# Kernel tuning notes

Hardware: AMD Instinct MI355X
Metric: run time of the kernel (lower is better)

The kernel has to match this reference:

```python
import jax, jax.numpy as jnp
import numpy as np

GROUPS = 32
K = 5          # up_kernel_size
UP = 2         # up_factor
EPS = 1e-5


def group_norm(x, w, b):
    B, C, H, W = x.shape
    xr = x.reshape(B, GROUPS, -1)
    mu = xr.mean(axis=2, keepdims=True)
    var = xr.var(axis=2, keepdims=True)
    xr = (xr - mu) * jax.lax.rsqrt(var + EPS)
    return xr.reshape(B, C, H, W) * w[None, :, None, None] + b[None, :, None, None]


def setup_inputs() -> dict:
    key = jax.random.key(0)
    ks = jax.random.split(key, 4)
    B, Cy, Cx, E, H, W = 4, 256, 256, 32, 64, 64
    return {
        "y": jax.random.normal(ks[0], (B, Cy, H * UP, W * UP), jnp.float32),
        "x": jax.random.normal(ks[1], (B, Cx, H, W), jnp.float32),
        "gn_y_w": jnp.ones((Cy,), jnp.float32),
        "gn_y_b": jnp.zeros((Cy,), jnp.float32),
        "gn_x_w": jnp.ones((Cx,), jnp.float32),
        "gn_x_b": jnp.zeros((Cx,), jnp.float32),
        "q_w": jax.random.normal(ks[2], (E, Cy), jnp.float32) * 0.02,
        "q_b": jnp.zeros((E,), jnp.float32),
        "k_w": jax.random.normal(ks[3], (E, Cx), jnp.float32) * 0.02,
        "k_b": jnp.zeros((E,), jnp.float32),
    }


def reference(y, x, gn_y_w, gn_y_b, gn_x_w, gn_x_b, q_w, q_b, k_w, k_b):
    pad = K // 2
    yn = group_norm(y, gn_y_w, gn_y_b)
    xn = group_norm(x, gn_x_w, gn_x_b)
    # 1x1 convs
    q = jnp.einsum('bchw,ec->behw', yn, q_w) + q_b[None, :, None, None]  # [B,E,Hu,Wu]
    k = jnp.einsum('bchw,ec->behw', xn, k_w) + k_b[None, :, None, None]  # [B,E,H,W]
    B, E, H, W = k.shape
    C = x.shape[1]
    # view q as per-low-res-cell blocks of UPxUP high-res queries
    q_r = q.reshape(B, E, H, UP, W, UP)
    k_pad = jnp.pad(k, ((0, 0), (0, 0), (pad, pad), (pad, pad)))  # zero pad (out-of-range -> 0 logit)
    v_pad = jnp.pad(x, ((0, 0), (0, 0), (pad, pad), (pad, pad)))
    # qk: logits over the KxK window (loop over 25 fixed offsets, vectorized inside)
    logits = []
    for dy in range(K):
        for dx in range(K):
            ks = k_pad[:, :, dy:dy + H, dx:dx + W]            # [B,E,H,W]
            logits.append(jnp.einsum('behuwv,behw->bhuwv', q_r, ks))
    logits = jnp.stack(logits, axis=1)                        # [B,KK,H,u,W,u]
    attn = jax.nn.softmax(logits, axis=1)
    # av: weighted aggregation of v over the same window
    out = jnp.zeros((B, C, H, UP, W, UP), x.dtype)
    idx = 0
    for dy in range(K):
        for dx in range(K):
            vs = v_pad[:, :, dy:dy + H, dx:dx + W]            # [B,C,H,W]
            out = out + attn[:, idx][:, None] * vs[:, :, :, None, :, None]
            idx += 1
    return out.reshape(B, C, H * UP, W * UP)
```

## Files before the change

### kernel.cpp

```cpp
#include <hip/hip_runtime.h>

#define EPSV 1e-5f

__global__ __launch_bounds__(256) void stats_kernel(const float* __restrict__ y,
                                                    const float* __restrict__ x,
                                                    float* __restrict__ part) {
    int bid = blockIdx.x;
    const float* src = (bid < 1024) ? (y + (size_t)bid * 16384)
                                    : (x + (size_t)(bid - 1024) * 16384);
    const float4* p = (const float4*)src;
    float s = 0.f, ss = 0.f;
    #pragma unroll 8
    for (int i = threadIdx.x; i < 4096; i += 256) {
        float4 v = p[i];
        s  += v.x + v.y + v.z + v.w;
        ss += v.x*v.x + v.y*v.y + v.z*v.z + v.w*v.w;
    }
    for (int off = 32; off > 0; off >>= 1) {
        s  += __shfl_down(s, off);
        ss += __shfl_down(ss, off);
    }
    __shared__ float red[8];
    int wid = threadIdx.x >> 6, lane = threadIdx.x & 63;
    if (lane == 0) { red[wid*2] = s; red[wid*2+1] = ss; }
    __syncthreads();
    if (threadIdx.x == 0) {
        part[bid*2+0] = red[0] + red[2] + red[4] + red[6];
        part[bid*2+1] = red[1] + red[3] + red[5] + red[7];
    }
}

__global__ __launch_bounds__(64) void make_eff_kernel(const float* __restrict__ qw, const float* __restrict__ qb,
                                                      const float* __restrict__ gyw, const float* __restrict__ gyb,
                                                      const float* __restrict__ kw, const float* __restrict__ kb,
                                                      const float* __restrict__ gxw, const float* __restrict__ gxb,
                                                      const float* __restrict__ part,
                                                      float* __restrict__ WeffQ, float* __restrict__ beffQ,
                                                      float* __restrict__ WeffK, float* __restrict__ beffK) {
    int id = blockIdx.x;
    int isK = id >> 7, b = (id >> 5) & 3, e = id & 31;
    const float* w     = isK ? kw  : qw;
    const float* bias  = isK ? kb  : qb;
    const float* gamma = isK ? gxw : gyw;
    const float* beta  = isK ? gxb : gyb;
    float inv_n = isK ? (1.f/32768.f) : (1.f/131072.f);
    float* W  = isK ? WeffK : WeffQ;
    float* be = isK ? beffK : beffQ;
    float partial = 0.f;
    for (int c = threadIdx.x; c < 256; c += 64) {
        int g = c >> 3, grp = b*32 + g;
        float s = 0.f, ss = 0.f;
        if (isK) {
            #pragma unroll
            for (int k2 = 0; k2 < 2; ++k2) {
                s  += part[(1024 + grp*2 + k2)*2 + 0];
                ss += part[(1024 + grp*2 + k2)*2 + 1];
            }
        } else {
            #pragma unroll
            for (int k2 = 0; k2 < 8; ++k2) {
                s  += part[(grp*8 + k2)*2 + 0];
                ss += part[(grp*8 + k2)*2 + 1];
            }
        }
        float mu = s * inv_n;
        float rs = rsqrtf(fmaf(-mu, mu, ss * inv_n) + EPSV);
        float wc = w[e*256 + c];
        float weff = wc * gamma[c] * rs;
        W[((size_t)b*256 + c)*32 + e] = weff;
        partial += wc * beta[c] - weff * mu;
    }
    for (int off = 32; off > 0; off >>= 1) partial += __shfl_down(partial, off);
    if (threadIdx.x == 0) be[b*32 + e] = partial + bias[e];
}

__global__ __launch_bounds__(256) void proj_kernel(const float* __restrict__ y, const float* __restrict__ x,
                                                   const float* __restrict__ WeffQ, const float* __restrict__ beffQ,
                                                   const float* __restrict__ WeffK, const float* __restrict__ beffK,
                                                   float* __restrict__ qbuf, float* __restrict__ kbuf) {
    int bid = blockIdx.x;
    int isX = bid >= 512;
    int lb = isX ? bid - 512 : bid;
    int b    = isX ? (lb >> 5) : (lb >> 7);
    int pxb  = isX ? (lb & 31) : (lb & 127);
    int npix = isX ? 4096 : 16384;
    const float* src   = isX ? x : y;
    const float* WeffT = isX ? WeffK : WeffQ;
    const float* beff  = isX ? beffK : beffQ;
    float* dst = isX ? kbuf : qbuf;

    int pix0 = pxb * 128 + (threadIdx.x & 63) * 2;
    int eg = __builtin_amdgcn_readfirstlane(threadIdx.x >> 6);
    const float* wp = WeffT + (size_t)b*256*32 + eg*8;
    float acc[2][8];
    #pragma unroll
    for (int j = 0; j < 8; ++j) {
        float bv = beff[b*32 + eg*8 + j];
        acc[0][j] = bv; acc[1][j] = bv;
    }
    const float* ysrc = src + (size_t)b*256*npix + pix0;
    #pragma unroll 8
    for (int c = 0; c < 256; ++c) {
        float2 t = *(const float2*)(ysrc + (size_t)c*npix);
        #pragma unroll
        for (int j = 0; j < 8; ++j) {
            float wj = wp[c*32 + j];
            acc[0][j] = fmaf(t.x, wj, acc[0][j]);
            acc[1][j] = fmaf(t.y, wj, acc[1][j]);
        }
    }
    float* dbase = dst + ((size_t)b*npix + pix0)*32 + eg*8;
    #pragma unroll
    for (int px = 0; px < 2; ++px) {
        float4 o0 = {acc[px][0], acc[px][1], acc[px][2], acc[px][3]};
        float4 o1 = {acc[px][4], acc[px][5], acc[px][6], acc[px][7]};
        *(float4*)(dbase + px*32 + 0) = o0;
        *(float4*)(dbase + px*32 + 4) = o1;
    }
}

__global__ __launch_bounds__(256) void attn_weights_kernel(const float* __restrict__ q,
                                                           const float* __restrict__ kk,
                                                           float* __restrict__ g_attn)
{
    __shared__ __align__(16) float sK[5184];
    __shared__ __align__(16) float sA[6400];
    int h0 = blockIdx.y * 8, w0 = blockIdx.x * 8;
    int b = blockIdx.z;
    int tid = threadIdx.x;

    for (int i = tid; i < 1152; i += 256) {
        int pos = i >> 3, e4 = i & 7;
        int r = pos / 12, c = pos - 12*r;
        int gh = h0 + r - 2, gw = w0 + c - 2;
        float4 v = make_float4(0.f, 0.f, 0.f, 0.f);
        if (gh >= 0 && gh < 64 && gw >= 0 && gw < 64)
            v = *(const float4*)(kk + (((size_t)b*4096 + gh*64 + gw)*32 + e4*4));
        *(float4*)&sK[pos*36 + e4*4] = v;
    }

    int h = tid >> 5, u = (tid >> 4) & 1, w = (tid >> 1) & 7, v = tid & 1;

    float qv[32];
    {
        int hh = 2*(h0 + h) + u, ww = 2*(w0 + w) + v;
        const float4* qp = (const float4*)(q + (((size_t)b*16384 + hh*128 + ww)*32));
        #pragma unroll
        for (int i4 = 0; i4 < 8; ++i4) {
            float4 t = qp[i4];
            qv[i4*4+0]=t.x; qv[i4*4+1]=t.y; qv[i4*4+2]=t.z; qv[i4*4+3]=t.w;
        }
    }
    __syncthreads();

    float a[25];
    const float* kbase = &sK[(h*12 + w)*36];
    #pragma unroll
    for (int j = 0; j < 25; ++j) {
        int dy = j / 5, dx = j - 5*dy;
        const float4* kp = (const float4*)(kbase + (dy*12 + dx)*36);
        float acc = 0.f;
        #pragma unroll
        for (int e4 = 0; e4 < 8; ++e4) {
            float4 kv = kp[e4];
            acc = fmaf(qv[e4*4+0], kv.x, acc);
            acc = fmaf(qv[e4*4+1], kv.y, acc);
            acc = fmaf(qv[e4*4+2], kv.z, acc);
            acc = fmaf(qv[e4*4+3], kv.w, acc);
        }
        a[j] = acc;
    }
    {
        float m = -1e30f;
        #pragma unroll
        for (int j = 0; j < 25; ++j) m = fmaxf(m, a[j]);
        float s = 0.f;
        #pragma unroll
        for (int j = 0; j < 25; ++j) { a[j] = __expf(a[j] - m); s += a[j]; }
        float inv = 1.f / s;
        #pragma unroll
        for (int j = 0; j < 25; ++j) sA[j*256 + tid] = a[j] * inv;
    }
    __syncthreads();

    float4* gdst = (float4*)(g_attn + ((size_t)b*64 + blockIdx.y*8 + blockIdx.x)*6400);
    const float4* ssrc = (const float4*)sA;
    for (int i = tid; i < 1600; i += 256) gdst[i] = ssrc[i];
}

__global__ __launch_bounds__(256) void gather_kernel(const float* __restrict__ g_attn,
                                                     const float* __restrict__ x,
                                                     float* __restrict__ out)
{
    __shared__ __align__(16) float sX[2880];
    int h0 = blockIdx.y * 8, w0 = blockIdx.x * 8;
    int b = blockIdx.z >> 4, chunk = blockIdx.z & 15;
    int tid = threadIdx.x;

    float a[25];
    {
        const float* abase = g_attn + ((size_t)b*64 + blockIdx.y*8 + blockIdx.x)*6400 + tid;
        #pragma unroll
        for (int j = 0; j < 25; ++j) a[j] = abase[j*256];
    }

    for (int i = 0; i < 9; ++i) {
        int t = i*256 + tid;
        int cc = t / 144, pos = t - 144*cc;
        int r = pos / 12, cl = pos - 12*r;
        int gh = h0 + r - 2, gw = w0 + cl - 2;
        float val = 0.f;
        if (gh >= 0 && gh < 64 && gw >= 0 && gw < 64)
            val = x[(((size_t)b*256 + chunk*16 + cc)*64 + gh)*64 + gw];
        sX[pos*20 + cc] = val;
    }

    int h = tid >> 5, u = (tid >> 4) & 1, w = (tid >> 1) & 7, v = tid & 1;
    int hh = 2*(h0 + h) + u, ww = 2*(w0 + w) + v;
    int vbase = (h*12 + w)*20;
    __syncthreads();

    #pragma unroll
    for (int g = 0; g < 4; ++g) {
        float o0 = 0.f, o1 = 0.f, o2 = 0.f, o3 = 0.f;
        const float* xb = &sX[vbase + g*4];
        #pragma unroll
        for (int j = 0; j < 25; ++j) {
            int dy = j / 5, dx = j - 5*dy;
            float4 xv = *(const float4*)(xb + (dy*12 + dx)*20);
            float aw = a[j];
            o0 = fmaf(aw, xv.x, o0);
            o1 = fmaf(aw, xv.y, o1);
            o2 = fmaf(aw, xv.z, o2);
            o3 = fmaf(aw, xv.w, o3);
        }
        size_t ob = (((size_t)b*256 + chunk*16 + g*4)*128 + hh)*128 + ww;
        out[ob]           = o0;
        out[ob + 16384]   = o1;
        out[ob + 32768]   = o2;
        out[ob + 49152]   = o3;
    }
}

extern "C" void kernel_launch(void* const* d_in, const int* in_sizes, int n_in,
                              void* d_out, int out_size, void* d_ws, size_t ws_size,
                              hipStream_t stream) {
    const float* y   = (const float*)d_in[0];
    const float* x   = (const float*)d_in[1];
    const float* gyw = (const float*)d_in[2];
    const float* gyb = (const float*)d_in[3];
    const float* gxw = (const float*)d_in[4];
    const float* gxb = (const float*)d_in[5];
    const float* qw  = (const float*)d_in[6];
    const float* qb  = (const float*)d_in[7];
    const float* kw  = (const float*)d_in[8];
    const float* kb  = (const float*)d_in[9];
    float* out = (float*)d_out;
    float* ws  = (float*)d_ws;

    float* part   = ws;
    float* WeffQ  = ws + 2560;
    float* beffQ  = ws + 35328;
    float* WeffK  = ws + 35456;
    float* beffK  = ws + 68224;
    float* qbuf   = ws + 68352;
    float* kbuf   = ws + 2165504;
    float* attnbf = ws + 2689792;

    stats_kernel<<<1280, 256, 0, stream>>>(y, x, part);
    make_eff_kernel<<<256, 64, 0, stream>>>(qw, qb, gyw, gyb, kw, kb, gxw, gxb,
                                            part, WeffQ, beffQ, WeffK, beffK);
    proj_kernel<<<640, 256, 0, stream>>>(y, x, WeffQ, beffQ, WeffK, beffK, qbuf, kbuf);
    attn_weights_kernel<<<dim3(8, 8, 4), 256, 0, stream>>>(qbuf, kbuf, attnbf);
    gather_kernel<<<dim3(8, 8, 64), 256, 0, stream>>>(attnbf, x, out);
}
```

Measured before the change: 204.2 us.

## Restructure projection to one pixel per thread and split attention dot over lanes

The projection kernel now uses 64-thread blocks where each thread computes all 32 output channels for one pixel. Each source element is loaded once and the weights become wave-uniform, replacing the earlier scheme of 8 channels by 2 pixels per thread. The attention-weights kernel doubles its threads per block, splits each 32-wide dot product across two half-waves and combines them with a cross-lane shuffle. It also writes softmax weights straight to global memory instead of staging them in shared memory. This is meant to add parallelism to the small 256-block attention launch and drop one LDS round trip and barrier, at the cost of more accumulator registers in the projection.

Result: slower. 221.1 us (+8.3%).

```diff
diff --git a/kernel.cpp b/kernel.cpp
--- a/kernel.cpp
+++ b/kernel.cpp
@@ -74,62 +74,54 @@
     if (threadIdx.x == 0) be[b*32 + e] = partial + bias[e];
 }
 
-__global__ __launch_bounds__(256) void proj_kernel(const float* __restrict__ y, const float* __restrict__ x,
-                                                   const float* __restrict__ WeffQ, const float* __restrict__ beffQ,
-                                                   const float* __restrict__ WeffK, const float* __restrict__ beffK,
-                                                   float* __restrict__ qbuf, float* __restrict__ kbuf) {
+__global__ __launch_bounds__(64) void proj_kernel(const float* __restrict__ y, const float* __restrict__ x,
+                                                  const float* __restrict__ WeffQ, const float* __restrict__ beffQ,
+                                                  const float* __restrict__ WeffK, const float* __restrict__ beffK,
+                                                  float* __restrict__ qbuf, float* __restrict__ kbuf) {
     int bid = blockIdx.x;
-    int isX = bid >= 512;
-    int lb = isX ? bid - 512 : bid;
-    int b    = isX ? (lb >> 5) : (lb >> 7);
-    int pxb  = isX ? (lb & 31) : (lb & 127);
+    int isX = bid >= 1024;
+    int lb  = isX ? bid - 1024 : bid;
+    int b   = isX ? (lb >> 6) : (lb >> 8);
+    int pxb = isX ? (lb & 63) : (lb & 255);
     int npix = isX ? 4096 : 16384;
     const float* src   = isX ? x : y;
     const float* WeffT = isX ? WeffK : WeffQ;
     const float* beff  = isX ? beffK : beffQ;
     float* dst = isX ? kbuf : qbuf;
 
-    int pix0 = pxb * 128 + (threadIdx.x & 63) * 2;
-    int eg = __builtin_amdgcn_readfirstlane(threadIdx.x >> 6);
-    const float* wp = WeffT + (size_t)b*256*32 + eg*8;
-    float acc[2][8];
-    #pragma unroll
-    for (int j = 0; j < 8; ++j) {
-        float bv = beff[b*32 + eg*8 + j];
-        acc[0][j] = bv; acc[1][j] = bv;
-    }
-    const float* ysrc = src + (size_t)b*256*npix + pix0;
-    #pragma unroll 8
+    int pix = pxb * 64 + threadIdx.x;
+    float acc[32];
+    #pragma unroll
+    for (int j = 0; j < 32; ++j) acc[j] = beff[b*32 + j];
+
+    const float* sp    = src + (size_t)b*256*npix + pix;
+    const float* wbase = WeffT + (size_t)b*256*32;
+    #pragma unroll 4
     for (int c = 0; c < 256; ++c) {
-        float2 t = *(const float2*)(ysrc + (size_t)c*npix);
-        #pragma unroll
-        for (int j = 0; j < 8; ++j) {
-            float wj = wp[c*32 + j];
-            acc[0][j] = fmaf(t.x, wj, acc[0][j]);
-            acc[1][j] = fmaf(t.y, wj, acc[1][j]);
-        }
-    }
-    float* dbase = dst + ((size_t)b*npix + pix0)*32 + eg*8;
-    #pragma unroll
-    for (int px = 0; px < 2; ++px) {
-        float4 o0 = {acc[px][0], acc[px][1], acc[px][2], acc[px][3]};
-        float4 o1 = {acc[px][4], acc[px][5], acc[px][6], acc[px][7]};
-        *(float4*)(dbase + px*32 + 0) = o0;
-        *(float4*)(dbase + px*32 + 4) = o1;
-    }
-}
-
-__global__ __launch_bounds__(256) void attn_weights_kernel(const float* __restrict__ q,
+        float t = sp[(size_t)c*npix];
+        const float* wc = wbase + c*32;
+        #pragma unroll
+        for (int j = 0; j < 32; ++j) acc[j] = fmaf(t, wc[j], acc[j]);
+    }
+
+    float* dbase = dst + ((size_t)b*npix + pix)*32;
+    #pragma unroll
+    for (int j4 = 0; j4 < 8; ++j4) {
+        float4 o = {acc[j4*4+0], acc[j4*4+1], acc[j4*4+2], acc[j4*4+3]};
+        *(float4*)(dbase + j4*4) = o;
+    }
+}
+
+__global__ __launch_bounds__(512) void attn_weights_kernel(const float* __restrict__ q,
                                                            const float* __restrict__ kk,
                                                            float* __restrict__ g_attn)
 {
     __shared__ __align__(16) float sK[5184];
-    __shared__ __align__(16) float sA[6400];
     int h0 = blockIdx.y * 8, w0 = blockIdx.x * 8;
     int b = blockIdx.z;
     int tid = threadIdx.x;
 
-    for (int i = tid; i < 1152; i += 256) {
+    for (int i = tid; i < 1152; i += 512) {
         int pos = i >> 3, e4 = i & 7;
         int r = pos / 12, c = pos - 12*r;
         int gh = h0 + r - 2, gw = w0 + c - 2;
@@ -139,14 +131,20 @@
         *(float4*)&sK[pos*36 + e4*4] = v;
     }
 
-    int h = tid >> 5, u = (tid >> 4) & 1, w = (tid >> 1) & 7, v = tid & 1;
-
-    float qv[32];
+    int wave = tid >> 6;
+    int lane = tid & 63;
+    int eq   = lane >> 5;
+    int cl   = lane & 31;
+    int child = wave*32 + cl;
+    int h = wave;
+    int u = (cl >> 4) & 1, w = (cl >> 1) & 7, v = cl & 1;
+
+    float qv[16];
     {
         int hh = 2*(h0 + h) + u, ww = 2*(w0 + w) + v;
-        const float4* qp = (const float4*)(q + (((size_t)b*16384 + hh*128 + ww)*32));
-        #pragma unroll
-        for (int i4 = 0; i4 < 8; ++i4) {
+        const float4* qp = (const float4*)(q + (((size_t)b*16384 + hh*128 + ww)*32 + eq*16));
+        #pragma unroll
+        for (int i4 = 0; i4 < 4; ++i4) {
             float4 t = qp[i4];
             qv[i4*4+0]=t.x; qv[i4*4+1]=t.y; qv[i4*4+2]=t.z; qv[i4*4+3]=t.w;
         }
@@ -154,14 +152,14 @@
     __syncthreads();
 
     float a[25];
-    const float* kbase = &sK[(h*12 + w)*36];
+    const float* kbase = &sK[(h*12 + w)*36 + eq*16];
     #pragma unroll
     for (int j = 0; j < 25; ++j) {
         int dy = j / 5, dx = j - 5*dy;
         const float4* kp = (const float4*)(kbase + (dy*12 + dx)*36);
         float acc = 0.f;
         #pragma unroll
-        for (int e4 = 0; e4 < 8; ++e4) {
+        for (int e4 = 0; e4 < 4; ++e4) {
             float4 kv = kp[e4];
             acc = fmaf(qv[e4*4+0], kv.x, acc);
             acc = fmaf(qv[e4*4+1], kv.y, acc);
@@ -170,22 +168,25 @@
         }
         a[j] = acc;
     }
-    {
-        float m = -1e30f;
-        #pragma unroll
-        for (int j = 0; j < 25; ++j) m = fmaxf(m, a[j]);
-        float s = 0.f;
-        #pragma unroll
-        for (int j = 0; j < 25; ++j) { a[j] = __expf(a[j] - m); s += a[j]; }
-        float inv = 1.f / s;
-        #pragma unroll
-        for (int j = 0; j < 25; ++j) sA[j*256 + tid] = a[j] * inv;
-    }
-    __syncthreads();
-
-    float4* gdst = (float4*)(g_attn + ((size_t)b*64 + blockIdx.y*8 + blockIdx.x)*6400);
-    const float4* ssrc = (const float4*)sA;
-    for (int i = tid; i < 1600; i += 256) gdst[i] = ssrc[i];
+    #pragma unroll
+    for (int j = 0; j < 25; ++j) a[j] += __shfl_xor(a[j], 32);
+
+    float m = -1e30f;
+    #pragma unroll
+    for (int j = 0; j < 25; ++j) m = fmaxf(m, a[j]);
+    float s = 0.f;
+    #pragma unroll
+    for (int j = 0; j < 25; ++j) { a[j] = __expf(a[j] - m); s += a[j]; }
+    float inv = 1.f / s;
+
+    float* gbase = g_attn + ((size_t)b*64 + blockIdx.y*8 + blockIdx.x)*6400 + child;
+    if (eq == 0) {
+        #pragma unroll
+        for (int jj = 0; jj < 13; ++jj) gbase[(2*jj)*256] = a[2*jj] * inv;
+    } else {
+        #pragma unroll
+        for (int jj = 0; jj < 12; ++jj) gbase[(2*jj+1)*256] = a[2*jj+1] * inv;
+    }
 }
 
 __global__ __launch_bounds__(256) void gather_kernel(const float* __restrict__ g_attn,
@@ -270,7 +271,7 @@
     stats_kernel<<<1280, 256, 0, stream>>>(y, x, part);
     make_eff_kernel<<<256, 64, 0, stream>>>(qw, qb, gyw, gyb, kw, kb, gxw, gxb,
                                             part, WeffQ, beffQ, WeffK, beffK);
-    proj_kernel<<<640, 256, 0, stream>>>(y, x, WeffQ, beffQ, WeffK, beffK, qbuf, kbuf);
-    attn_weights_kernel<<<dim3(8, 8, 4), 256, 0, stream>>>(qbuf, kbuf, attnbf);
+    proj_kernel<<<1280, 64, 0, stream>>>(y, x, WeffQ, beffQ, WeffK, beffK, qbuf, kbuf);
+    attn_weights_kernel<<<dim3(8, 8, 4), 512, 0, stream>>>(qbuf, kbuf, attnbf);
     gather_kernel<<<dim3(8, 8, 64), 256, 0, stream>>>(attnbf, x, out);
 }
```
